# Performance work log

Hardware: AMD Instinct MI355X
Metric: run time of the kernel (lower is better)

The kernel has to match this reference:

```python
import jax, jax.numpy as jnp
import numpy as np

B = 16      # graphs
NPG = 1024  # nodes per graph (equal-sized, contiguous)
N = B * NPG
K = 12      # knn neighbors
DM = 128    # d_model
DH = 256    # d_hidden = 2*d_model
L = 3       # num_layers
DI = 2 * DM + 4  # msg mlp input dim


def _mlp2(x, W1, b1, W2, b2):
    return jax.nn.silu(x @ W1 + b1) @ W2 + b2


def setup_inputs() -> dict:
    key = jax.random.key(0)
    ks = list(jax.random.split(key, 16))
    def nrm(k, shape, fan):
        return jax.random.normal(k, shape, jnp.float32) / np.float32(np.sqrt(fan))
    return dict(
        x=jax.random.normal(ks[0], (N, 3), jnp.float32),
        batch=(jnp.arange(N) // NPG).astype(jnp.int32),
        in_W1=nrm(ks[1], (3, DM), 3), in_b1=jnp.zeros((DM,), jnp.float32),
        in_W2=nrm(ks[2], (DM, DM), DM), in_b2=jnp.zeros((DM,), jnp.float32),
        msg_W1=nrm(ks[3], (L, DI, DH), DI), msg_b1=jnp.zeros((L, DH), jnp.float32),
        msg_W2=nrm(ks[4], (L, DH, DM), DH), msg_b2=jnp.zeros((L, DM), jnp.float32),
        upd_W1=nrm(ks[5], (L, 2 * DM, DH), 2 * DM), upd_b1=jnp.zeros((L, DH), jnp.float32),
        upd_W2=nrm(ks[6], (L, DH, DM), DH), upd_b2=jnp.zeros((L, DM), jnp.float32),
        norm_w=jnp.ones((L, DM), jnp.float32), norm_b=jnp.zeros((L, DM), jnp.float32),
        norm_ms=jnp.ones((L, DM), jnp.float32),
        gate_W1=nrm(ks[7], (DM, DM), DM), gate_b1=jnp.zeros((DM,), jnp.float32),
        gate_W2=nrm(ks[8], (DM, 1), DM), gate_b2=jnp.zeros((1,), jnp.float32),
        head_W1=nrm(ks[9], (DM, DM), DM), head_b1=jnp.zeros((DM,), jnp.float32),
        head_W2=nrm(ks[10], (DM, 1), DM), head_b2=jnp.zeros((1,), jnp.float32),
    )


def _knn_edges(pos):
    # pos: [N,2]; graphs are contiguous blocks of NPG nodes -> blocked knn
    p3 = pos.reshape(B, NPG, 2)
    d2 = jnp.sum((p3[:, :, None, :] - p3[:, None, :, :]) ** 2, axis=-1)  # [B,n,n]
    d2 = jnp.where(jnp.eye(NPG, dtype=bool)[None], jnp.inf, d2)          # no self loops
    idx = jax.lax.top_k(-d2, K)[1]  # [B,n,K] nearest neighbors (sources)
    offs = (jnp.arange(B) * NPG)[:, None, None]
    src = (idx + offs).reshape(-1)
    dst = jnp.broadcast_to(jnp.arange(N).reshape(B, NPG, 1), (B, NPG, K)).reshape(-1)
    return src, dst


def _graph_norm(h, batch, cnt, w, b, ms):
    # PyG GraphNorm: out = w * (h - ms*mean) / sqrt(var + eps) + b, per-graph stats
    mean = jax.ops.segment_sum(h, batch, B) / cnt
    out = h - mean[batch] * ms
    var = jax.ops.segment_sum(out ** 2, batch, B) / cnt
    return w * out / jnp.sqrt(var + 1e-5)[batch] + b


def _forward(x, batch, in_W1, in_b1, in_W2, in_b2, msg_W1, msg_b1, msg_W2, msg_b2,
             upd_W1, upd_b1, upd_W2, upd_b2, norm_w, norm_b, norm_ms,
             gate_W1, gate_b1, gate_W2, gate_b2, head_W1, head_b1, head_W2, head_b2):
    pos = x[:, 1:3]
    src, dst = _knn_edges(pos)
    # edge_attr = [dx, dy, dist, ds]
    dp = pos[src] - pos[dst]
    dist = jnp.sqrt(jnp.sum(dp ** 2, axis=-1, keepdims=True) + 1e-12)
    ds = x[src, 0:1] - x[dst, 0:1]
    ea = jnp.concatenate([dp, dist, ds], axis=-1)  # [E,4]

    h = _mlp2(x, in_W1, in_b1, in_W2, in_b2)       # [N,DM]
    cnt = jax.ops.segment_sum(jnp.ones((N,), h.dtype), batch, B)[:, None]

    for i in range(L):
        m_in = jnp.concatenate([h[dst], h[src], ea], axis=-1)       # [E,2*DM+4]
        m = _mlp2(m_in, msg_W1[i], msg_b1[i], msg_W2[i], msg_b2[i])  # [E,DM]
        agg = jax.ops.segment_sum(m, dst, N)                         # scatter_add
        dh = _mlp2(jnp.concatenate([h, agg], axis=-1),
                   upd_W1[i], upd_b1[i], upd_W2[i], upd_b2[i])
        h = h + dh  # dropout is identity at inference
        h = _graph_norm(h, batch, cnt, norm_w[i], norm_b[i], norm_ms[i])

    # gated attention pool: segment softmax over gate logits
    gl = (jnp.tanh(h @ gate_W1 + gate_b1) @ gate_W2 + gate_b2)[:, 0]  # [N]
    gmax = jax.ops.segment_max(gl, batch, B)
    e = jnp.exp(gl - gmax[batch])
    a = e / jax.ops.segment_sum(e, batch, B)[batch]
    pooled = jax.ops.segment_sum(h * a[:, None], batch, B)            # [B,DM]

    return _mlp2(pooled, head_W1, head_b1, head_W2, head_b2)[:, 0]    # [B]


def reference(x, batch, in_W1, in_b1, in_W2, in_b2, msg_W1, msg_b1, msg_W2, msg_b2,
              upd_W1, upd_b1, upd_W2, upd_b2, norm_w, norm_b, norm_ms,
              gate_W1, gate_b1, gate_W2, gate_b2, head_W1, head_b1, head_W2, head_b2):
    return _forward(x, batch, in_W1, in_b1, in_W2, in_b2, msg_W1, msg_b1, msg_W2, msg_b2,
                    upd_W1, upd_b1, upd_W2, upd_b2, norm_w, norm_b, norm_ms,
                    gate_W1, gate_b1, gate_W2, gate_b2, head_W1, head_b1, head_W2, head_b2)
```

## Files before the change

### kernel.cpp

```cpp
#include <hip/hip_runtime.h>
#include <math.h>

#define NPTS 16384
#define BGR 16
#define NPGR 1024
#define KNN 12
#define DM 128
#define DH 256
#define NL 3
#define EDG (NPTS*KNN)

typedef unsigned short u16;
typedef unsigned int u32;
typedef __attribute__((ext_vector_type(8))) short short8;
typedef __attribute__((ext_vector_type(4))) float floatx4;

__device__ __forceinline__ float silu_f(float x) {
    return x / (1.0f + __expf(-x));
}
__device__ __forceinline__ u16 f2bf(float f) {
    union { float f; u32 u; } v; v.f = f;
    u32 r = v.u + 0x7fffu + ((v.u >> 16) & 1u);
    return (u16)(r >> 16);
}
__device__ __forceinline__ float bf2f(u16 b) {
    union { u32 u; float f; } v; v.u = ((u32)b) << 16;
    return v.f;
}
__device__ __forceinline__ void glds16(const u16* gp, u16* lp) {
    __builtin_amdgcn_global_load_lds(
        (const __attribute__((address_space(1))) void*)gp,
        (__attribute__((address_space(3))) void*)lp, 16, 0, 0);
}
__device__ __forceinline__ int lofs(int row, int q) {
    return row * 32 + ((q ^ ((row >> 2) & 3)) << 3);
}

#define KPPB 32
__global__ __launch_bounds__(256) void knn_kernel(const float* __restrict__ x,
                                                  int* __restrict__ srcb,
                                                  float* __restrict__ ea) {
#pragma clang fp contract(off)
    __shared__ float2 pxy[NPGR];
    __shared__ float s0[NPGR];
    __shared__ float sdf[256 * 13];
    __shared__ int   sif[256 * 13];
    __shared__ int   sel[KPPB][KNN];
    int t = threadIdx.x;
    int g   = blockIdx.x / (NPGR / KPPB);
    int blk = blockIdx.x % (NPGR / KPPB);
    int base = g * NPGR;
    for (int j = t; j < NPGR; j += 256) {
        const float* xp = x + (size_t)(base + j) * 3;
        s0[j] = xp[0];
        pxy[j] = make_float2(xp[1], xp[2]);
    }
    __syncthreads();
    int r  = t & 7;
    int pt = t >> 3;
    int il = blk * KPPB + pt;
    float2 pil = pxy[il];
    float xi = pil.x, yi = pil.y;
    float nd[KNN]; int ni[KNN];
#pragma unroll
    for (int k = 0; k < KNN; ++k) { nd[k] = 3.4e38f; ni[k] = 0x7fffffff; }
    for (int jj = 0; jj < 128; ++jj) {
        int j = jj * 8 + r;
        if (j == il) continue;
        float2 p = pxy[j];
        float dx = p.x - xi;
        float dy = p.y - yi;
        float dx2 = dx * dx;
        float dy2 = dy * dy;
        float d2 = dx2 + dy2;
        if (d2 < nd[KNN-1]) {
            float cd = d2; int ci = j;
#pragma unroll
            for (int k = 0; k < KNN; ++k) {
                bool sw = cd < nd[k];
                float tdv = sw ? nd[k] : cd;
                nd[k] = sw ? cd : nd[k];
                cd = tdv;
                int tiv = sw ? ni[k] : ci;
                ni[k] = sw ? ci : ni[k];
                ci = tiv;
            }
        }
    }
    int li = pt * 8 + r;
#pragma unroll
    for (int k = 0; k < KNN; ++k) {
        sdf[li * 13 + k] = nd[k];
        sif[li * 13 + k] = ni[k];
    }
    __syncthreads();
    if (r == 0) {
        int head[8];
#pragma unroll
        for (int q = 0; q < 8; ++q) head[q] = 0;
#pragma unroll
        for (int k = 0; k < KNN; ++k) {
            float bd = 3.4e38f; int bi = 0x7fffffff; int bq = 0;
#pragma unroll
            for (int q = 0; q < 8; ++q) {
                int hq = head[q];
                float d = (hq < KNN) ? sdf[(pt * 8 + q) * 13 + hq] : 3.4e38f;
                int  ix = (hq < KNN) ? sif[(pt * 8 + q) * 13 + hq] : 0x7fffffff;
                if (d < bd || (d == bd && ix < bi)) { bd = d; bi = ix; bq = q; }
            }
            head[bq]++;
            sel[pt][k] = bi;
        }
    }
    __syncthreads();
    float x0i = s0[il];
    for (int k = r; k < KNN; k += 8) {
        int j = sel[pt][k];
        size_t e = (size_t)(base + il) * KNN + k;
        srcb[e] = base + j;
        float2 pj = pxy[j];
        float dpx = pj.x - xi, dpy = pj.y - yi;
        float a = dpx * dpx;
        float b = dpy * dpy;
        float dist = sqrtf(a + b + 1e-12f);
        float dsv = s0[j] - x0i;
        *(float4*)(ea + e * 4) = make_float4(dpx, dpy, dist, dsv);
    }
}

__global__ __launch_bounds__(128) void in_mlp_kernel(const float* __restrict__ x,
    const float* __restrict__ W1, const float* __restrict__ b1,
    const float* __restrict__ W2, const float* __restrict__ b2,
    float* __restrict__ h, u16* __restrict__ hh, u16* __restrict__ hl) {
    __shared__ float hid[8][DM];
    __shared__ float xl[8][3];
    int t = threadIdx.x;
    int nb = blockIdx.x * 8;
    if (t < 24) xl[t / 3][t % 3] = x[(size_t)nb * 3 + t];
    __syncthreads();
    float w0 = W1[t], w1 = W1[DM + t], w2 = W1[2 * DM + t], bb = b1[t];
#pragma unroll
    for (int gi = 0; gi < 8; ++gi) {
        float v = xl[gi][0] * w0 + xl[gi][1] * w1 + xl[gi][2] * w2 + bb;
        hid[gi][t] = silu_f(v);
    }
    __syncthreads();
    float acc[8];
    float b2v = b2[t];
#pragma unroll
    for (int gi = 0; gi < 8; ++gi) acc[gi] = b2v;
    for (int k = 0; k < DM; ++k) {
        float w = W2[k * DM + t];
#pragma unroll
        for (int gi = 0; gi < 8; ++gi) acc[gi] += hid[gi][k] * w;
    }
#pragma unroll
    for (int gi = 0; gi < 8; ++gi) {
        size_t idx = (size_t)(nb + gi) * DM + t;
        float v = acc[gi];
        h[idx] = v;
        u16 hi = f2bf(v);
        hh[idx] = hi;
        hl[idx] = f2bf(v - bf2f(hi));
    }
}

#define MBM 64
#define MBN 128
#define MBK 32

__global__ __launch_bounds__(256) void mgemm_kernel(
    const u16* __restrict__ A0h, const u16* __restrict__ A0l, int k0, int lda0,
    const u16* __restrict__ A1h, const u16* __restrict__ A1l, int lda1,
    const u16* __restrict__ Wh, const u16* __restrict__ Wl, int K,
    const float* __restrict__ bias, int biasN,
    const float* __restrict__ resid, int ldres,
    float* __restrict__ outf, u16* __restrict__ outh, u16* __restrict__ outl, int ldout,
    int act)
{
    __shared__ __align__(16) u16 Ash[MBM * 32];
    __shared__ __align__(16) u16 Asl[MBM * 32];
    __shared__ __align__(16) u16 Bsh[MBN * 32];
    __shared__ __align__(16) u16 Bsl[MBN * 32];
    int t = threadIdx.x;
    int row0 = blockIdx.x * MBM, col0 = blockIdx.y * MBN;
    int lane = t & 63, w = t >> 6;
    int wm = (w >> 1) * 32, wn = (w & 1) * 64;
    int quad = lane >> 4, r15 = lane & 15;
    int rowl = lane >> 2, slot = lane & 3;

    floatx4 acc[2][4];
#pragma unroll
    for (int m = 0; m < 2; ++m)
#pragma unroll
        for (int n = 0; n < 4; ++n) acc[m][n] = (floatx4){0.f, 0.f, 0.f, 0.f};

    for (int kt = 0; kt < K; kt += MBK) {
        const u16 *Abh, *Abl; int lda, ko;
        if (kt < k0) { Abh = A0h; Abl = A0l; lda = lda0; ko = kt; }
        else         { Abh = A1h; Abl = A1l; lda = lda1; ko = kt - k0; }
        __syncthreads();
        {
            int ra = w * 16 + rowl;
            int gca = (slot ^ ((ra >> 2) & 3)) << 3;
            size_t aoff = (size_t)(row0 + ra) * lda + ko + gca;
            glds16(Abh + aoff, Ash + w * 16 * 32);
            glds16(Abl + aoff, Asl + w * 16 * 32);
            int rb0 = w * 32 + rowl;
            int gc0 = (slot ^ ((rb0 >> 2) & 3)) << 3;
            size_t boff0 = (size_t)(col0 + rb0) * K + kt + gc0;
            glds16(Wh + boff0, Bsh + w * 32 * 32);
            glds16(Wl + boff0, Bsl + w * 32 * 32);
            int rb1 = rb0 + 16;
            int gc1 = (slot ^ ((rb1 >> 2) & 3)) << 3;
            size_t boff1 = (size_t)(col0 + rb1) * K + kt + gc1;
            glds16(Wh + boff1, Bsh + (w * 32 + 16) * 32);
            glds16(Wl + boff1, Bsl + (w * 32 + 16) * 32);
        }
        __syncthreads();
        short8 ah[2], alo[2], bhf[4], blf[4];
#pragma unroll
        for (int m = 0; m < 2; ++m) {
            int off = lofs(wm + m * 16 + r15, quad);
            ah[m]  = *(const short8*)(Ash + off);
            alo[m] = *(const short8*)(Asl + off);
        }
#pragma unroll
        for (int n = 0; n < 4; ++n) {
            int off = lofs(wn + n * 16 + r15, quad);
            bhf[n] = *(const short8*)(Bsh + off);
            blf[n] = *(const short8*)(Bsl + off);
        }
#pragma unroll
        for (int m = 0; m < 2; ++m)
#pragma unroll
            for (int n = 0; n < 4; ++n) {
                acc[m][n] = __builtin_amdgcn_mfma_f32_16x16x32_bf16(ah[m],  bhf[n], acc[m][n], 0, 0, 0);
                acc[m][n] = __builtin_amdgcn_mfma_f32_16x16x32_bf16(ah[m],  blf[n], acc[m][n], 0, 0, 0);
                acc[m][n] = __builtin_amdgcn_mfma_f32_16x16x32_bf16(alo[m], bhf[n], acc[m][n], 0, 0, 0);
            }
    }
#pragma unroll
    for (int n = 0; n < 4; ++n) {
        int col = col0 + wn + n*16 + r15;
        float bv = (bias && col < biasN) ? bias[col] : 0.f;
#pragma unroll
        for (int m = 0; m < 2; ++m) {
#pragma unroll
            for (int reg = 0; reg < 4; ++reg) {
                int row = row0 + wm + m*16 + quad*4 + reg;
                float v = acc[m][n][reg] + bv;
                if (act == 1) v = silu_f(v);
                else if (act == 2) v = tanhf(v);
                if (resid) v += resid[(size_t)row * ldres + col];
                size_t oidx = (size_t)row * ldout + col;
                if (outf) outf[oidx] = v;
                if (outh) {
                    u16 hi = f2bf(v);
                    outh[oidx] = hi;
                    outl[oidx] = f2bf(v - bf2f(hi));
                }
            }
        }
    }
}

#define M2BM 128
__global__ __launch_bounds__(256) void mgemm128_kernel(
    const u16* __restrict__ A0h, const u16* __restrict__ A0l, int k0, int lda0,
    const u16* __restrict__ A1h, const u16* __restrict__ A1l, int lda1,
    const u16* __restrict__ Wh, const u16* __restrict__ Wl, int K,
    const float* __restrict__ bias, int biasN,
    float* __restrict__ outf, u16* __restrict__ outh, u16* __restrict__ outl, int ldout,
    int act)
{
    __shared__ __align__(16) u16 Ash[M2BM * 32];
    __shared__ __align__(16) u16 Asl[M2BM * 32];
    __shared__ __align__(16) u16 Bsh[MBN * 32];
    __shared__ __align__(16) u16 Bsl[MBN * 32];
    int t = threadIdx.x;
    int row0 = blockIdx.x * M2BM, col0 = blockIdx.y * MBN;
    int lane = t & 63, w = t >> 6;
    int wm = (w >> 1) * 64, wn = (w & 1) * 64;
    int quad = lane >> 4, r15 = lane & 15;
    int rowl = lane >> 2, slot = lane & 3;

    floatx4 acc[4][4];
#pragma unroll
    for (int m = 0; m < 4; ++m)
#pragma unroll
        for (int n = 0; n < 4; ++n) acc[m][n] = (floatx4){0.f, 0.f, 0.f, 0.f};

    for (int kt = 0; kt < K; kt += MBK) {
        const u16 *Abh, *Abl; int lda, ko;
        if (kt < k0) { Abh = A0h; Abl = A0l; lda = lda0; ko = kt; }
        else         { Abh = A1h; Abl = A1l; lda = lda1; ko = kt - k0; }
        __syncthreads();
        {
            int ra0 = w * 32 + rowl;
            int gca0 = (slot ^ ((ra0 >> 2) & 3)) << 3;
            size_t aoff0 = (size_t)(row0 + ra0) * lda + ko + gca0;
            glds16(Abh + aoff0, Ash + w * 32 * 32);
            glds16(Abl + aoff0, Asl + w * 32 * 32);
            int ra1 = ra0 + 16;
            int gca1 = (slot ^ ((ra1 >> 2) & 3)) << 3;
            size_t aoff1 = (size_t)(row0 + ra1) * lda + ko + gca1;
            glds16(Abh + aoff1, Ash + (w * 32 + 16) * 32);
            glds16(Abl + aoff1, Asl + (w * 32 + 16) * 32);
            int rb0 = w * 32 + rowl;
            int gcb0 = (slot ^ ((rb0 >> 2) & 3)) << 3;
            size_t boff0 = (size_t)(col0 + rb0) * K + kt + gcb0;
            glds16(Wh + boff0, Bsh + w * 32 * 32);
            glds16(Wl + boff0, Bsl + w * 32 * 32);
            int rb1 = rb0 + 16;
            int gcb1 = (slot ^ ((rb1 >> 2) & 3)) << 3;
            size_t boff1 = (size_t)(col0 + rb1) * K + kt + gcb1;
            glds16(Wh + boff1, Bsh + (w * 32 + 16) * 32);
            glds16(Wl + boff1, Bsl + (w * 32 + 16) * 32);
        }
        __syncthreads();
        short8 ah[4], alo[4], bhf[4], blf[4];
#pragma unroll
        for (int m = 0; m < 4; ++m) {
            int off = lofs(wm + m * 16 + r15, quad);
            ah[m]  = *(const short8*)(Ash + off);
            alo[m] = *(const short8*)(Asl + off);
        }
#pragma unroll
        for (int n = 0; n < 4; ++n) {
            int off = lofs(wn + n * 16 + r15, quad);
            bhf[n] = *(const short8*)(Bsh + off);
            blf[n] = *(const short8*)(Bsl + off);
        }
#pragma unroll
        for (int m = 0; m < 4; ++m)
#pragma unroll
            for (int n = 0; n < 4; ++n) {
                acc[m][n] = __builtin_amdgcn_mfma_f32_16x16x32_bf16(ah[m],  bhf[n], acc[m][n], 0, 0, 0);
                acc[m][n] = __builtin_amdgcn_mfma_f32_16x16x32_bf16(ah[m],  blf[n], acc[m][n], 0, 0, 0);
                acc[m][n] = __builtin_amdgcn_mfma_f32_16x16x32_bf16(alo[m], bhf[n], acc[m][n], 0, 0, 0);
            }
    }
#pragma unroll
    for (int n = 0; n < 4; ++n) {
        int col = col0 + wn + n*16 + r15;
        float bv = (bias && col < biasN) ? bias[col] : 0.f;
#pragma unroll
        for (int m = 0; m < 4; ++m) {
#pragma unroll
            for (int reg = 0; reg < 4; ++reg) {
                int row = row0 + wm + m*16 + quad*4 + reg;
                float v = acc[m][n][reg] + bv;
                if (act == 1) v = silu_f(v);
                size_t oidx = (size_t)row * ldout + col;
                if (outf) outf[oidx] = v;
                if (outh) {
                    u16 hi = f2bf(v);
                    outh[oidx] = hi;
                    outl[oidx] = f2bf(v - bf2f(hi));
                }
            }
        }
    }
}

__global__ __launch_bounds__(256) void edge_agg_kernel(
    const float* __restrict__ CS,
    const int* __restrict__ srcb, const float* __restrict__ ea,
    const float* __restrict__ W1ea,
    u16* __restrict__ HSh, u16* __restrict__ HSl)
{
    int i = blockIdx.x, t = threadIdx.x;
    __shared__ int ss[KNN];
    __shared__ float sea[KNN * 4];
    if (t < KNN) ss[t] = srcb[(size_t)i * KNN + t];
    if (t < KNN * 4) sea[t] = ea[(size_t)i * KNN * 4 + t];
    __syncthreads();
    float base = CS[(size_t)i * 512 + t];
    float wa = W1ea[t], wb = W1ea[DH + t], wc = W1ea[2 * DH + t], wd = W1ea[3 * DH + t];
    float hs = 0.f;
#pragma unroll
    for (int e = 0; e < KNN; ++e) {
        float v = base + CS[(size_t)ss[e] * 512 + 256 + t]
                + sea[e * 4 + 0] * wa + sea[e * 4 + 1] * wb
                + sea[e * 4 + 2] * wc + sea[e * 4 + 3] * wd;
        hs += silu_f(v);
    }
    size_t oidx = (size_t)i * DH + t;
    u16 hi = f2bf(hs);
    HSh[oidx] = hi;
    HSl[oidx] = f2bf(hs - bf2f(hi));
}

__global__ __launch_bounds__(256) void norm_part_kernel(const float* __restrict__ hn,
                                                        float* __restrict__ psum)
{
    int g = blockIdx.x, blk = blockIdx.y;
    int t = threadIdx.x, d = t & 127, half = t >> 7;
    size_t base = ((size_t)g * NPGR + (size_t)blk * 128 + half * 64) * DM;
    float s = 0.f, s2 = 0.f;
    for (int n = 0; n < 64; ++n) {
        float v = hn[base + (size_t)n * DM + d];
        s += v; s2 += v * v;
    }
    __shared__ float ps[2][DM], ps2[2][DM];
    ps[half][d] = s; ps2[half][d] = s2;
    __syncthreads();
    if (t < DM) {
        psum[(((size_t)g * 8 + blk) * 2 + 0) * DM + d] = ps[0][d] + ps[1][d];
        psum[(((size_t)g * 8 + blk) * 2 + 1) * DM + d] = ps2[0][d] + ps2[1][d];
    }
}

__global__ __launch_bounds__(256) void norm_apply_kernel(const float* __restrict__ hn,
    float* __restrict__ h, u16* __restrict__ hh, u16* __restrict__ hl,
    const float* __restrict__ psum,
    const float* __restrict__ w, const float* __restrict__ b, const float* __restrict__ ms)
{
    int g = blockIdx.x, blk = blockIdx.y, t = threadIdx.x;
    __shared__ float mmv[DM], rst[DM], wv[DM], bv[DM];
    if (t < DM) {
        float sum = 0.f, sq = 0.f;
        for (int q = 0; q < 8; ++q) {
            sum += psum[(((size_t)g * 8 + q) * 2 + 0) * DM + t];
            sq  += psum[(((size_t)g * 8 + q) * 2 + 1) * DM + t];
        }
        float mean = sum * (1.0f / NPGR);
        float mm = mean * ms[t];
        float var = sq * (1.0f / NPGR) - 2.f * mm * mean + mm * mm;
        mmv[t] = mm;
        rst[t] = 1.0f / sqrtf(var + 1e-5f);
        wv[t] = w[t]; bv[t] = b[t];
    }
    __syncthreads();
    size_t base = ((size_t)g * NPGR + (size_t)blk * 128) * DM;
    for (int i = t; i < 128 * DM; i += 256) {
        int dd = i & 127;
        float v = hn[base + i];
        float o = wv[dd] * (v - mmv[dd]) * rst[dd] + bv[dd];
        h[base + i] = o;
        u16 hi = f2bf(o);
        hh[base + i] = hi;
        hl[base + i] = f2bf(o - bf2f(hi));
    }
}

__global__ __launch_bounds__(256) void gate_dot_kernel(const float* __restrict__ Gh,
    const float* __restrict__ gW2, const float* __restrict__ gb2,
    float* __restrict__ gl)
{
    int t = threadIdx.x, lane = t & 63, w = t >> 6;
    int node = blockIdx.x * 4 + w;
    const float* gp = Gh + (size_t)node * DM;
    float v = gp[lane] * gW2[lane] + gp[lane + 64] * gW2[lane + 64];
    for (int off = 32; off > 0; off >>= 1) v += __shfl_down(v, off, 64);
    if (lane == 0) gl[node] = v + gb2[0];
}

__global__ __launch_bounds__(256) void pool_stats_kernel(const float* __restrict__ gl,
                                                         float* __restrict__ gstat)
{
    int g = blockIdx.x, t = threadIdx.x, lane = t & 63, w = t >> 6;
    __shared__ float red[4];
    const float* gp = gl + (size_t)g * NPGR;
    float mx = -3.4e38f;
    for (int n = t; n < NPGR; n += 256) mx = fmaxf(mx, gp[n]);
    for (int off = 32; off > 0; off >>= 1) mx = fmaxf(mx, __shfl_down(mx, off, 64));
    if (lane == 0) red[w] = mx;
    __syncthreads();
    float gmax = fmaxf(fmaxf(red[0], red[1]), fmaxf(red[2], red[3]));
    __syncthreads();
    float se = 0.f;
    for (int n = t; n < NPGR; n += 256) se += __expf(gp[n] - gmax);
    for (int off = 32; off > 0; off >>= 1) se += __shfl_down(se, off, 64);
    if (lane == 0) red[w] = se;
    __syncthreads();
    if (t == 0) { gstat[g * 2] = gmax; gstat[g * 2 + 1] = red[0] + red[1] + red[2] + red[3]; }
}

__global__ __launch_bounds__(256) void pool_part_kernel(const float* __restrict__ h,
    const float* __restrict__ gl, const float* __restrict__ gstat,
    float* __restrict__ ppool)
{
    int g = blockIdx.x, blk = blockIdx.y;
    int t = threadIdx.x, d = t & 127, half = t >> 7;
    float gmax = gstat[g * 2];
    size_t nbase = (size_t)g * NPGR + (size_t)blk * 128 + half * 64;
    float p = 0.f;
    for (int n = 0; n < 64; ++n)
        p += __expf(gl[nbase + n] - gmax) * h[(nbase + n) * DM + d];
    __shared__ float ps[2][DM];
    ps[half][d] = p;
    __syncthreads();
    if (t < DM) ppool[((size_t)g * 8 + blk) * DM + d] = ps[0][d] + ps[1][d];
}

__global__ __launch_bounds__(128) void pool_head_kernel(const float* __restrict__ ppool,
    const float* __restrict__ gstat,
    const float* __restrict__ hW1, const float* __restrict__ hb1,
    const float* __restrict__ hW2, const float* __restrict__ hb2,
    float* __restrict__ outp)
{
    int g = blockIdx.x, t = threadIdx.x;
    __shared__ float pl[DM];
    __shared__ float red[2];
    float ssum = gstat[g * 2 + 1];
    float p = 0.f;
    for (int q = 0; q < 8; ++q) p += ppool[((size_t)g * 8 + q) * DM + t];
    pl[t] = p / ssum;
    __syncthreads();
    float a = hb1[t];
    for (int k = 0; k < DM; ++k) a += pl[k] * hW1[k * DM + t];
    a = silu_f(a);
    float vv = a * hW2[t];
    int lane = t & 63, w = t >> 6;
    for (int off = 32; off > 0; off >>= 1) vv += __shfl_down(vv, off, 64);
    if (lane == 0) red[w] = vv;
    __syncthreads();
    if (t == 0) outp[g] = red[0] + red[1] + hb2[0];
}

__global__ __launch_bounds__(256) void precompute_kernel(
    const float* __restrict__ msgW2, const float* __restrict__ msgb2,
    const float* __restrict__ updW1, const float* __restrict__ updb1,
    float* __restrict__ W2U, float* __restrict__ bias2)
{
    int bid = blockIdx.x; int t = threadIdx.x;
    if (bid < NL * DH) {
        int l = bid / DH, k = bid % DH;
        const float* w2row = msgW2 + (size_t)l * DH * DM + (size_t)k * DM;
        const float* u1 = updW1 + (size_t)l * 2 * DM * DH;
        float acc = 0.f;
        for (int j = 0; j < DM; ++j) acc += w2row[j] * u1[(size_t)(DM + j) * DH + t];
        W2U[(size_t)l * DH * DH + (size_t)k * DH + t] = acc;
    } else {
        int l = bid - NL * DH;
        const float* u1 = updW1 + (size_t)l * 2 * DM * DH;
        const float* b2 = msgb2 + (size_t)l * DM;
        float acc = updb1[(size_t)l * DH + t];
        for (int j = 0; j < DM; ++j) acc += 12.0f * b2[j] * u1[(size_t)(DM + j) * DH + t];
        bias2[(size_t)l * DH + t] = acc;
    }
}

struct WJob { const float* src; u16* dh; u16* dl; int K, N, ldd, off; };
struct WJobs { WJob j[16]; };
__global__ __launch_bounds__(256) void wprep_kernel(WJobs jobs) {
    WJob jb = jobs.j[blockIdx.y];
    int n = blockIdx.x;
    if (n >= jb.N) return;
    for (int k = threadIdx.x; k < jb.K; k += 256) {
        float v = jb.src[(size_t)k * jb.N + n];
        u16 hi = f2bf(v);
        u16 lo = f2bf(v - bf2f(hi));
        jb.dh[(size_t)n * jb.ldd + jb.off + k] = hi;
        jb.dl[(size_t)n * jb.ldd + jb.off + k] = lo;
    }
}

extern "C" void kernel_launch(void* const* d_in, const int* in_sizes, int n_in,
                              void* d_out, int out_size, void* d_ws, size_t ws_size,
                              hipStream_t stream) {
    const float* x     = (const float*)d_in[0];
    const float* inW1  = (const float*)d_in[2];
    const float* inb1  = (const float*)d_in[3];
    const float* inW2  = (const float*)d_in[4];
    const float* inb2  = (const float*)d_in[5];
    const float* msgW1 = (const float*)d_in[6];
    const float* msgb1 = (const float*)d_in[7];
    const float* msgW2 = (const float*)d_in[8];
    const float* msgb2 = (const float*)d_in[9];
    const float* updW1 = (const float*)d_in[10];
    const float* updb1 = (const float*)d_in[11];
    const float* updW2 = (const float*)d_in[12];
    const float* updb2 = (const float*)d_in[13];
    const float* nw    = (const float*)d_in[14];
    const float* nb    = (const float*)d_in[15];
    const float* nms   = (const float*)d_in[16];
    const float* gW1   = (const float*)d_in[17];
    const float* gb1   = (const float*)d_in[18];
    const float* gW2   = (const float*)d_in[19];
    const float* gb2   = (const float*)d_in[20];
    const float* hW1   = (const float*)d_in[21];
    const float* hb1   = (const float*)d_in[22];
    const float* hW2   = (const float*)d_in[23];
    const float* hb2   = (const float*)d_in[24];
    float* outp = (float*)d_out;

    float* ws    = (float*)d_ws;
    float* h     = ws;
    float* CSb   = h + (size_t)NPTS * DM;
    float* hnb   = CSb + (size_t)NPTS * 512;
    float* W2U   = hnb + (size_t)NPTS * DM;
    float* bias2 = W2U + (size_t)NL * DH * DH;
    float* glb   = bias2 + NL * DH;
    int*   srcb  = (int*)(glb + NPTS);
    float* eab   = (float*)(srcb + EDG);
    float* psum  = eab + (size_t)EDG * 4;
    float* gstat = psum + 16 * 8 * 2 * DM;
    float* ppool = gstat + 32;
    u16* hh  = (u16*)(ppool + 16 * 8 * DM);
    u16* hl  = hh + (size_t)NPTS * DM;
    u16* HSh = hl + (size_t)NPTS * DM;
    u16* HSl = HSh + (size_t)NPTS * DH;
    u16* Th  = HSl + (size_t)NPTS * DH;
    u16* Tl  = Th + (size_t)NPTS * DH;
    u16* WCSh = Tl + (size_t)NPTS * DH;              u16* WCSl = WCSh + (size_t)NL * 512 * DM;
    u16* WTh = WCSl + (size_t)NL * 512 * DM;         u16* WTl = WTh + (size_t)NL * DH * 384;
    u16* WUh = WTl + (size_t)NL * DH * 384;          u16* WUl = WUh + (size_t)NL * DM * DH;
    u16* WGh = WUl + (size_t)NL * DM * DH;           u16* WGl = WGh + (size_t)DM * DM;

    hipLaunchKernelGGL(precompute_kernel, dim3(NL * DH + NL), dim3(DH), 0, stream,
                       msgW2, msgb2, updW1, updb1, W2U, bias2);

    WJobs jobs;
    int ji = 0;
    for (int l = 0; l < NL; ++l) {
        jobs.j[ji++] = WJob{ msgW1 + (size_t)l * 260 * DH,            WCSh + (size_t)l * 512 * DM,            WCSl + (size_t)l * 512 * DM,            128, 256, 128, 0 };
        jobs.j[ji++] = WJob{ msgW1 + (size_t)l * 260 * DH + 128 * DH, WCSh + (size_t)l * 512 * DM + 256 * DM, WCSl + (size_t)l * 512 * DM + 256 * DM, 128, 256, 128, 0 };
        jobs.j[ji++] = WJob{ updW1 + (size_t)l * 256 * DH,            WTh + (size_t)l * DH * 384, WTl + (size_t)l * DH * 384, 128, 256, 384, 0 };
        jobs.j[ji++] = WJob{ W2U   + (size_t)l * DH * DH,             WTh + (size_t)l * DH * 384, WTl + (size_t)l * DH * 384, 256, 256, 384, 128 };
        jobs.j[ji++] = WJob{ updW2 + (size_t)l * DH * DM,             WUh + (size_t)l * DM * DH, WUl + (size_t)l * DM * DH, 256, 128, 256, 0 };
    }
    jobs.j[ji++] = WJob{ gW1, WGh, WGl, 128, 128, 128, 0 };
    hipLaunchKernelGGL(wprep_kernel, dim3(256, 16), dim3(256), 0, stream, jobs);

    hipLaunchKernelGGL(knn_kernel, dim3(NPTS / KPPB), dim3(256), 0, stream, x, srcb, eab);
    hipLaunchKernelGGL(in_mlp_kernel, dim3(NPTS / 8), dim3(128), 0, stream,
                       x, inW1, inb1, inW2, inb2, h, hh, hl);

    for (int l = 0; l < NL; ++l) {
        const float* W1l = msgW1 + (size_t)l * 260 * DH;
        hipLaunchKernelGGL(mgemm128_kernel, dim3(NPTS / M2BM, 512 / MBN), dim3(256), 0, stream,
            hh, hl, DM, DM, (const u16*)nullptr, (const u16*)nullptr, 0,
            WCSh + (size_t)l * 512 * DM, WCSl + (size_t)l * 512 * DM, DM,
            msgb1 + (size_t)l * DH, 256,
            CSb, (u16*)nullptr, (u16*)nullptr, 512, 0);
        hipLaunchKernelGGL(edge_agg_kernel, dim3(NPTS), dim3(DH), 0, stream,
            CSb, srcb, eab, W1l + (size_t)2 * DM * DH, HSh, HSl);
        hipLaunchKernelGGL(mgemm_kernel, dim3(NPTS / MBM, DH / MBN), dim3(256), 0, stream,
            hh, hl, DM, DM, HSh, HSl, DH,
            WTh + (size_t)l * DH * 384, WTl + (size_t)l * DH * 384, 384,
            bias2 + (size_t)l * DH, DH, (const float*)nullptr, 0,
            (float*)nullptr, Th, Tl, DH, 1);
        hipLaunchKernelGGL(mgemm_kernel, dim3(NPTS / MBM, DM / MBN), dim3(256), 0, stream,
            Th, Tl, DH, DH, (const u16*)nullptr, (const u16*)nullptr, 0,
            WUh + (size_t)l * DM * DH, WUl + (size_t)l * DM * DH, DH,
            updb2 + (size_t)l * DM, DM, h, DM,
            hnb, (u16*)nullptr, (u16*)nullptr, DM, 0);
        hipLaunchKernelGGL(norm_part_kernel, dim3(BGR, 8), dim3(256), 0, stream, hnb, psum);
        hipLaunchKernelGGL(norm_apply_kernel, dim3(BGR, 8), dim3(256), 0, stream,
            hnb, h, hh, hl, psum, nw + (size_t)l * DM, nb + (size_t)l * DM, nms + (size_t)l * DM);
    }

    hipLaunchKernelGGL(mgemm_kernel, dim3(NPTS / MBM, DM / MBN), dim3(256), 0, stream,
        hh, hl, DM, DM, (const u16*)nullptr, (const u16*)nullptr, 0,
        WGh, WGl, DM, gb1, DM, (const float*)nullptr, 0,
        hnb, (u16*)nullptr, (u16*)nullptr, DM, 2);
    hipLaunchKernelGGL(gate_dot_kernel, dim3(NPTS / 4), dim3(256), 0, stream,
        hnb, gW2, gb2, glb);

    hipLaunchKernelGGL(pool_stats_kernel, dim3(BGR), dim3(256), 0, stream, glb, gstat);
    hipLaunchKernelGGL(pool_part_kernel, dim3(BGR, 8), dim3(256), 0, stream, h, glb, gstat, ppool);
    hipLaunchKernelGGL(pool_head_kernel, dim3(BGR), dim3(128), 0, stream,
        ppool, gstat, hW1, hb1, hW2, hb2, outp);
}
```

Baseline: 539.5 us.

## Fuse GraphNorm partial sums into GEMM epilogue, batch edge agg, tile weight transpose

The update GEMM epilogue now accumulates per-column sum and sum-of-squares over its 64-row tile and writes partial statistics, which removes the separate norm_part kernel and its re-read of hnb. The norm_apply kernel now reads 16 chunks per graph instead of 8. The edge aggregation kernel handles 4 nodes per block to amortise the index and edge-attribute loads. The weight prep kernel uses a shared-memory tiled transpose so its global reads and writes are coalesced. The fused epilogue adds shuffles and a block barrier to every GEMM tile that computes statistics.

```diff
diff --git a/kernel.cpp b/kernel.cpp
--- a/kernel.cpp
+++ b/kernel.cpp
@@ -176,12 +176,13 @@
     const float* __restrict__ bias, int biasN,
     const float* __restrict__ resid, int ldres,
     float* __restrict__ outf, u16* __restrict__ outh, u16* __restrict__ outl, int ldout,
-    int act)
+    int act, float* __restrict__ psum)
 {
     __shared__ __align__(16) u16 Ash[MBM * 32];
     __shared__ __align__(16) u16 Asl[MBM * 32];
     __shared__ __align__(16) u16 Bsh[MBN * 32];
     __shared__ __align__(16) u16 Bsl[MBN * 32];
+    __shared__ float partS[4][64], partS2[4][64];
     int t = threadIdx.x;
     int row0 = blockIdx.x * MBM, col0 = blockIdx.y * MBN;
     int lane = t & 63, w = t >> 6;
@@ -240,10 +241,12 @@
                 acc[m][n] = __builtin_amdgcn_mfma_f32_16x16x32_bf16(alo[m], bhf[n], acc[m][n], 0, 0, 0);
             }
     }
+    float cs[4], cs2[4];
 #pragma unroll
     for (int n = 0; n < 4; ++n) {
         int col = col0 + wn + n*16 + r15;
         float bv = (bias && col < biasN) ? bias[col] : 0.f;
+        float s1 = 0.f, sq = 0.f;
 #pragma unroll
         for (int m = 0; m < 2; ++m) {
 #pragma unroll
@@ -260,7 +263,28 @@
                     outh[oidx] = hi;
                     outl[oidx] = f2bf(v - bf2f(hi));
                 }
+                if (psum) { s1 += v; sq += v * v; }
             }
+        }
+        cs[n] = s1; cs2[n] = sq;
+    }
+    if (psum) {
+#pragma unroll
+        for (int n = 0; n < 4; ++n) {
+            float s1 = cs[n], sq = cs2[n];
+            s1 += __shfl_xor(s1, 16, 64); s1 += __shfl_xor(s1, 32, 64);
+            sq += __shfl_xor(sq, 16, 64); sq += __shfl_xor(sq, 32, 64);
+            if (quad == 0) { partS[w][n*16 + r15] = s1; partS2[w][n*16 + r15] = sq; }
+        }
+        __syncthreads();
+        if (t < 128) {
+            int colg = t >> 6, ci = t & 63;
+            float s1 = partS[colg][ci] + partS[colg + 2][ci];
+            float sq = partS2[colg][ci] + partS2[colg + 2][ci];
+            int col = colg * 64 + ci;
+            int g = row0 >> 10, chunk = (row0 & 1023) >> 6;
+            psum[(((size_t)g * 16 + chunk) * 2 + 0) * DM + col] = s1;
+            psum[(((size_t)g * 16 + chunk) * 2 + 1) * DM + col] = sq;
         }
     }
 }
@@ -364,51 +388,36 @@
     }
 }
 
+#define EPB 4
 __global__ __launch_bounds__(256) void edge_agg_kernel(
     const float* __restrict__ CS,
     const int* __restrict__ srcb, const float* __restrict__ ea,
     const float* __restrict__ W1ea,
     u16* __restrict__ HSh, u16* __restrict__ HSl)
 {
-    int i = blockIdx.x, t = threadIdx.x;
-    __shared__ int ss[KNN];
-    __shared__ float sea[KNN * 4];
-    if (t < KNN) ss[t] = srcb[(size_t)i * KNN + t];
-    if (t < KNN * 4) sea[t] = ea[(size_t)i * KNN * 4 + t];
-    __syncthreads();
-    float base = CS[(size_t)i * 512 + t];
+    int i0 = blockIdx.x * EPB, t = threadIdx.x;
+    __shared__ int ss[EPB][KNN];
+    __shared__ float sea[EPB][KNN * 4];
+    if (t < EPB * KNN) ss[t / KNN][t % KNN] = srcb[(size_t)i0 * KNN + t];
+    if (t < EPB * KNN * 4) sea[t / (KNN * 4)][t % (KNN * 4)] = ea[(size_t)i0 * KNN * 4 + t];
+    __syncthreads();
     float wa = W1ea[t], wb = W1ea[DH + t], wc = W1ea[2 * DH + t], wd = W1ea[3 * DH + t];
-    float hs = 0.f;
-#pragma unroll
-    for (int e = 0; e < KNN; ++e) {
-        float v = base + CS[(size_t)ss[e] * 512 + 256 + t]
-                + sea[e * 4 + 0] * wa + sea[e * 4 + 1] * wb
-                + sea[e * 4 + 2] * wc + sea[e * 4 + 3] * wd;
-        hs += silu_f(v);
-    }
-    size_t oidx = (size_t)i * DH + t;
-    u16 hi = f2bf(hs);
-    HSh[oidx] = hi;
-    HSl[oidx] = f2bf(hs - bf2f(hi));
-}
-
-__global__ __launch_bounds__(256) void norm_part_kernel(const float* __restrict__ hn,
-                                                        float* __restrict__ psum)
-{
-    int g = blockIdx.x, blk = blockIdx.y;
-    int t = threadIdx.x, d = t & 127, half = t >> 7;
-    size_t base = ((size_t)g * NPGR + (size_t)blk * 128 + half * 64) * DM;
-    float s = 0.f, s2 = 0.f;
-    for (int n = 0; n < 64; ++n) {
-        float v = hn[base + (size_t)n * DM + d];
-        s += v; s2 += v * v;
-    }
-    __shared__ float ps[2][DM], ps2[2][DM];
-    ps[half][d] = s; ps2[half][d] = s2;
-    __syncthreads();
-    if (t < DM) {
-        psum[(((size_t)g * 8 + blk) * 2 + 0) * DM + d] = ps[0][d] + ps[1][d];
-        psum[(((size_t)g * 8 + blk) * 2 + 1) * DM + d] = ps2[0][d] + ps2[1][d];
+#pragma unroll
+    for (int v4 = 0; v4 < EPB; ++v4) {
+        int i = i0 + v4;
+        float base = CS[(size_t)i * 512 + t];
+        float hs = 0.f;
+#pragma unroll
+        for (int e = 0; e < KNN; ++e) {
+            float v = base + CS[(size_t)ss[v4][e] * 512 + 256 + t]
+                    + sea[v4][e * 4 + 0] * wa + sea[v4][e * 4 + 1] * wb
+                    + sea[v4][e * 4 + 2] * wc + sea[v4][e * 4 + 3] * wd;
+            hs += silu_f(v);
+        }
+        size_t oidx = (size_t)i * DH + t;
+        u16 hi = f2bf(hs);
+        HSh[oidx] = hi;
+        HSl[oidx] = f2bf(hs - bf2f(hi));
     }
 }
 
@@ -421,9 +430,9 @@
     __shared__ float mmv[DM], rst[DM], wv[DM], bv[DM];
     if (t < DM) {
         float sum = 0.f, sq = 0.f;
-        for (int q = 0; q < 8; ++q) {
-            sum += psum[(((size_t)g * 8 + q) * 2 + 0) * DM + t];
-            sq  += psum[(((size_t)g * 8 + q) * 2 + 1) * DM + t];
+        for (int q = 0; q < 16; ++q) {
+            sum += psum[(((size_t)g * 16 + q) * 2 + 0) * DM + t];
+            sq  += psum[(((size_t)g * 16 + q) * 2 + 1) * DM + t];
         }
         float mean = sum * (1.0f / NPGR);
         float mm = mean * ms[t];
@@ -547,14 +556,26 @@
 struct WJobs { WJob j[16]; };
 __global__ __launch_bounds__(256) void wprep_kernel(WJobs jobs) {
     WJob jb = jobs.j[blockIdx.y];
-    int n = blockIdx.x;
-    if (n >= jb.N) return;
-    for (int k = threadIdx.x; k < jb.K; k += 256) {
-        float v = jb.src[(size_t)k * jb.N + n];
-        u16 hi = f2bf(v);
-        u16 lo = f2bf(v - bf2f(hi));
-        jb.dh[(size_t)n * jb.ldd + jb.off + k] = hi;
-        jb.dl[(size_t)n * jb.ldd + jb.off + k] = lo;
+    int tiles_k = (jb.K + 31) / 32, tiles_n = (jb.N + 31) / 32;
+    int tile = blockIdx.x;
+    if (tile >= tiles_k * tiles_n) return;
+    int kt = (tile % tiles_k) * 32, nt = (tile / tiles_k) * 32;
+    __shared__ float tl[32][33];
+    int i = threadIdx.x >> 5, j = threadIdx.x & 31;
+    for (int r = i; r < 32; r += 8) {
+        int k = kt + r, n = nt + j;
+        if (k < jb.K && n < jb.N) tl[r][j] = jb.src[(size_t)k * jb.N + n];
+    }
+    __syncthreads();
+    for (int r = i; r < 32; r += 8) {
+        int n = nt + r, k = kt + j;
+        if (n < jb.N && k < jb.K) {
+            float v = tl[j][r];
+            u16 hi = f2bf(v);
+            u16 lo = f2bf(v - bf2f(hi));
+            jb.dh[(size_t)n * jb.ldd + jb.off + k] = hi;
+            jb.dl[(size_t)n * jb.ldd + jb.off + k] = lo;
+        }
     }
 }
 
@@ -597,7 +618,7 @@
     int*   srcb  = (int*)(glb + NPTS);
     float* eab   = (float*)(srcb + EDG);
     float* psum  = eab + (size_t)EDG * 4;
-    float* gstat = psum + 16 * 8 * 2 * DM;
+    float* gstat = psum + 16 * 16 * 2 * DM;
     float* ppool = gstat + 32;
     u16* hh  = (u16*)(ppool + 16 * 8 * DM);
     u16* hl  = hh + (size_t)NPTS * DM;
@@ -623,7 +644,7 @@
         jobs.j[ji++] = WJob{ updW2 + (size_t)l * DH * DM,             WUh + (size_t)l * DM * DH, WUl + (size_t)l * DM * DH, 256, 128, 256, 0 };
     }
     jobs.j[ji++] = WJob{ gW1, WGh, WGl, 128, 128, 128, 0 };
-    hipLaunchKernelGGL(wprep_kernel, dim3(256, 16), dim3(256), 0, stream, jobs);
+    hipLaunchKernelGGL(wprep_kernel, dim3(64, 16), dim3(256), 0, stream, jobs);
 
     hipLaunchKernelGGL(knn_kernel, dim3(NPTS / KPPB), dim3(256), 0, stream, x, srcb, eab);
     hipLaunchKernelGGL(in_mlp_kernel, dim3(NPTS / 8), dim3(128), 0, stream,
@@ -636,19 +657,18 @@
             WCSh + (size_t)l * 512 * DM, WCSl + (size_t)l * 512 * DM, DM,
             msgb1 + (size_t)l * DH, 256,
             CSb, (u16*)nullptr, (u16*)nullptr, 512, 0);
-        hipLaunchKernelGGL(edge_agg_kernel, dim3(NPTS), dim3(DH), 0, stream,
+        hipLaunchKernelGGL(edge_agg_kernel, dim3(NPTS / EPB), dim3(DH), 0, stream,
             CSb, srcb, eab, W1l + (size_t)2 * DM * DH, HSh, HSl);
         hipLaunchKernelGGL(mgemm_kernel, dim3(NPTS / MBM, DH / MBN), dim3(256), 0, stream,
             hh, hl, DM, DM, HSh, HSl, DH,
             WTh + (size_t)l * DH * 384, WTl + (size_t)l * DH * 384, 384,
             bias2 + (size_t)l * DH, DH, (const float*)nullptr, 0,
-            (float*)nullptr, Th, Tl, DH, 1);
+            (float*)nullptr, Th, Tl, DH, 1, (float*)nullptr);
         hipLaunchKernelGGL(mgemm_kernel, dim3(NPTS / MBM, DM / MBN), dim3(256), 0, stream,
             Th, Tl, DH, DH, (const u16*)nullptr, (const u16*)nullptr, 0,
             WUh + (size_t)l * DM * DH, WUl + (size_t)l * DM * DH, DH,
             updb2 + (size_t)l * DM, DM, h, DM,
-            hnb, (u16*)nullptr, (u16*)nullptr, DM, 0);
-        hipLaunchKernelGGL(norm_part_kernel, dim3(BGR, 8), dim3(256), 0, stream, hnb, psum);
+            hnb, (u16*)nullptr, (u16*)nullptr, DM, 0, psum);
         hipLaunchKernelGGL(norm_apply_kernel, dim3(BGR, 8), dim3(256), 0, stream,
             hnb, h, hh, hl, psum, nw + (size_t)l * DM, nb + (size_t)l * DM, nms + (size_t)l * DM);
     }
@@ -656,7 +676,7 @@
     hipLaunchKernelGGL(mgemm_kernel, dim3(NPTS / MBM, DM / MBN), dim3(256), 0, stream,
         hh, hl, DM, DM, (const u16*)nullptr, (const u16*)nullptr, 0,
         WGh, WGl, DM, gb1, DM, (const float*)nullptr, 0,
-        hnb, (u16*)nullptr, (u16*)nullptr, DM, 2);
+        hnb, (u16*)nullptr, (u16*)nullptr, DM, 2, (float*)nullptr);
     hipLaunchKernelGGL(gate_dot_kernel, dim3(NPTS / 4), dim3(256), 0, stream,
         hnb, gW2, gb2, glb);
 
```

Result: no change. 543.5 us (+0.7%).
